# Optimization experiments

Hardware: AMD Instinct MI355X
Metric: run time of the kernel (lower is better)

The kernel has to match this reference:

```python
import jax, jax.numpy as jnp
import numpy as np

B, G, N_IN, N_HID, N_OUT = 2, 4096, 8, 32, 32
ALPHA, BETA, BN_EPS = 0.005, 5e-5, 1e-5
EDGE_P = 0.05  # adjacency density


def _lin_init(k, fan_in, fan_out):
    k1, k2 = jax.random.split(k)
    lim = 1.0 / np.sqrt(fan_in)
    W = jax.random.uniform(k1, (fan_in, fan_out), minval=-lim, maxval=lim, dtype=jnp.float32)
    b = jax.random.uniform(k2, (fan_out,), minval=-lim, maxval=lim, dtype=jnp.float32)
    return W, b


def setup_inputs() -> dict:
    key = jax.random.key(0)
    ks = jax.random.split(key, 12)
    W_infer, b_infer = _lin_init(ks[0], N_IN, N_HID)
    W_e1, b_e1 = _lin_init(ks[1], 2 * N_HID, 1)
    W_e2, b_e2 = _lin_init(ks[2], 2 * N_HID, 1)
    W_n1, b_n1 = _lin_init(ks[3], 2 * N_HID, N_OUT)
    W_n2, b_n2 = _lin_init(ks[4], 2 * N_HID, N_OUT)
    W_m1, b_m1 = _lin_init(ks[5], 2 * N_HID, N_OUT)
    W_m2, b_m2 = _lin_init(ks[6], 2 * N_HID, N_OUT)
    x = jax.random.normal(ks[7], (B, G, N_IN), dtype=jnp.float32)
    edges1 = jax.random.bernoulli(ks[8], EDGE_P, (G, G)).astype(jnp.float32)
    edges2 = jax.random.bernoulli(ks[9], EDGE_P, (G, G)).astype(jnp.float32)
    bn_gamma = jnp.ones((G,), jnp.float32)
    bn_beta = jnp.zeros((G,), jnp.float32)
    return dict(x=x, edges1=edges1, edges2=edges2, W_infer=W_infer, b_infer=b_infer,
                W_e1=W_e1, b_e1=b_e1, W_e2=W_e2, b_e2=b_e2,
                W_n1=W_n1, b_n1=b_n1, W_n2=W_n2, b_n2=b_n2,
                W_m1=W_m1, b_m1=b_m1, W_m2=W_m2, b_m2=b_m2,
                bn_gamma=bn_gamma, bn_beta=bn_beta)


def _mp_block(x, adj, coef, W_e, b_e, W_n, b_n, W_m, b_m):
    # x: [B,G,H]. Torch builds edge feature at flat index k=i*G+j as cat([x_j, x_i])
    # (shape2 = col gather, shape1 = row gather). We keep the same math without
    # materializing the [B,G*G,2H] tensor.
    Hh = x.shape[-1]
    s_src = x @ W_e[:Hh]   # [B,G,1]  (x_j part of mlp_edge)
    s_dst = x @ W_e[Hh:]   # [B,G,1]  (x_i part of mlp_edge)
    logits = s_dst[:, :, None, 0] + s_src[:, None, :, 0] + b_e[0]   # [B,G,G] at (i,j)
    w = adj + coef * (adj == 0).astype(x.dtype)                     # ori_edge + coef*thres_edge
    e = jax.nn.sigmoid(logits) * w[None]                            # [B,G,G]
    # receive at node i: sum_j e_ij * [x_j, x_i]
    recv_src = jnp.einsum('bij,bjh->bih', e, x)                     # sum_j e_ij x_j
    recv_dst = x * jnp.sum(e, axis=2)[..., None]                    # x_i * sum_j e_ij
    recv = jnp.concatenate([recv_src, recv_dst], axis=-1)           # [B,G,2H]
    recv = jax.nn.elu(recv @ W_n + b_n)                             # nodes_mlp + elu
    upd = jnp.concatenate([recv, x], axis=-1) @ W_m + b_m           # mesg_merge (mode='cat')
    return jax.nn.elu(upd)


def _forward(x, edges1, edges2, W_infer, b_infer, W_e1, b_e1, W_e2, b_e2,
             W_n1, b_n1, W_n2, b_n2, W_m1, b_m1, W_m2, b_m2, bn_gamma, bn_beta):
    h = jax.nn.elu(x @ W_infer + b_infer)                           # infer + elu, [B,G,H]
    h = _mp_block(h, edges1, ALPHA, W_e1, b_e1, W_n1, b_n1, W_m1, b_m1)
    # BatchNorm1d(gene_num) on [B, G, n_out]: per-gene stats over (batch, feature)
    mu = jnp.mean(h, axis=(0, 2), keepdims=True)
    var = jnp.var(h, axis=(0, 2), keepdims=True)
    h = (h - mu) * jax.lax.rsqrt(var + BN_EPS)
    h = h * bn_gamma[None, :, None] + bn_beta[None, :, None]
    return _mp_block(h, edges2, BETA, W_e2, b_e2, W_n2, b_n2, W_m2, b_m2)


def reference(x, edges1, edges2, W_infer, b_infer, W_e1, b_e1, W_e2, b_e2,
              W_n1, b_n1, W_n2, b_n2, W_m1, b_m1, W_m2, b_m2, bn_gamma, bn_beta):
    return _forward(x, edges1, edges2, W_infer, b_infer, W_e1, b_e1, W_e2, b_e2,
                    W_n1, b_n1, W_n2, b_n2, W_m1, b_m1, W_m2, b_m2, bn_gamma, bn_beta)
```

## Files before the change

### kernel.cpp

```cpp
#include <hip/hip_runtime.h>

#define G 4096
#define BSZ 2
#define NIN 8
#define HID 32
#define NLOG2E (-1.4426950408889634f)

typedef __attribute__((ext_vector_type(8))) short short8;
typedef __attribute__((ext_vector_type(4))) float floatx4;
typedef unsigned short ushort_t;
typedef unsigned int uint_t;

__device__ __forceinline__ float elu1(float v) {
    return v > 0.f ? v : (__expf(v) - 1.f);
}
__device__ __forceinline__ ushort_t f2bf(float f) {
    unsigned u = __float_as_uint(f);
    u += 0x7fffu + ((u >> 16) & 1u);
    return (ushort_t)(u >> 16);
}

__global__ __launch_bounds__(256) void k_setup1(
    const float* __restrict__ x, const float* __restrict__ W,
    const float* __restrict__ bias, const float* __restrict__ We,
    float* __restrict__ h0, ushort_t* __restrict__ hTb,
    float* __restrict__ ssrc, float* __restrict__ sdst) {
    __shared__ __align__(16) ushort_t hs[HID][264];
    int tid = threadIdx.x;
    int t = blockIdx.x * 256 + tid;
    int b = t >> 12;
    int g0 = (blockIdx.x & 15) * 256;
    float xin[NIN];
    const float* xp = x + t * NIN;
#pragma unroll
    for (int k = 0; k < NIN; k++) xin[k] = xp[k];
    float ss = 0.f, sd = 0.f;
    float* hp = h0 + (size_t)t * HID;
#pragma unroll
    for (int o = 0; o < HID; o++) {
        float v = bias[o];
#pragma unroll
        for (int k = 0; k < NIN; k++) v += xin[k] * W[k * HID + o];
        v = elu1(v);
        hp[o] = v;
        hs[o][tid] = f2bf(v);
        ss += v * We[o];
        sd += v * We[HID + o];
    }
    ssrc[t] = ss * NLOG2E;
    sdst[t] = sd * NLOG2E;
    __syncthreads();
#pragma unroll
    for (int p = 0; p < 4; p++) {
        int row = p * 8 + (tid >> 5);
        int c = (tid & 31) * 8;
        short8 v8 = *(const short8*)&hs[row][c];
        *(short8*)(void*)&hTb[(size_t)(b * HID + row) * G + g0 + c] = v8;
    }
}

template <bool DO_BN>
__global__ __launch_bounds__(1024, 4) void k_fused(
    const float* __restrict__ adj, const float* __restrict__ ssrc,
    const float* __restrict__ sdst, const ushort_t* __restrict__ hTb_in,
    const float* __restrict__ bep, float coef, const float* __restrict__ hin,
    const float* __restrict__ Wn, const float* __restrict__ bnb,
    const float* __restrict__ Wm, const float* __restrict__ bmb,
    const float* __restrict__ gamma, const float* __restrict__ beta,
    const float* __restrict__ We2, float* __restrict__ outp,
    ushort_t* __restrict__ hTb_out, float* __restrict__ s2s,
    float* __restrict__ s2d) {
    union SMemU {
        float ssm[BSZ][G];
        struct {
            float rec[32][68];
            float rec2[32][68];
            float esg[16][2];
            ushort_t tb[BSZ][HID][16];
        } p;
    };
    __shared__ __align__(16) SMemU sm;
    __shared__ __align__(16) uint_t abits[128][16];
    __shared__ __align__(16) float red[14][64][9];
    __shared__ __align__(16) float Wns[2048];
    __shared__ __align__(16) float Wms[2048];

    int tid = threadIdx.x;
    int g0 = blockIdx.x * 16;
    int l = tid & 63, w = tid >> 6;
    int b = w >> 3, jq = w & 7;

    if (tid < 512) {
        ((float4*)Wns)[tid] = ((const float4*)Wn)[tid];
    } else {
        int t2 = tid - 512;
        ((float4*)Wms)[t2] = ((const float4*)Wm)[t2];
    }
#pragma unroll
    for (int r = 0; r < 2; r++) {
        int idx = r * 4096 + tid * 4;
        int bb = idx >> 12, j = idx & 4095;
        *(float4*)&sm.ssm[bb][j] = *(const float4*)&ssrc[bb * G + j];
    }

    int m = l & 15, kg = l >> 4;
    int jstart = jq * 512;
    const ushort_t* hb0 = hTb_in + (size_t)(b * HID + m) * G + jstart + kg * 8;
    const ushort_t* hb1 = hb0 + (size_t)16 * G;
    short8 pb0[4], pb1[4];
#pragma unroll
    for (int d = 0; d < 4; d++) {
        pb0[d] = *(const short8*)(const void*)(hb0 + d * 32);
        pb1[d] = *(const short8*)(const void*)(hb1 + d * 32);
    }

    {
        int jw = tid >> 3;
        bool st = (tid & 7) == 0;
        int sh2 = (tid & 7) * 4;
        float4 ld[8];
#pragma unroll
        for (int h = 0; h < 2; h++) {
#pragma unroll
            for (int s = 0; s < 8; s++)
                ld[s] = *(const float4*)&adj[(size_t)(g0 + h * 8 + s) * G + tid * 4];
#pragma unroll
            for (int s = 0; s < 8; s++) {
                float4 v4 = ld[s];
                uint_t nib = (uint_t)(v4.x != 0.f) | ((uint_t)(v4.y != 0.f) << 1) |
                             ((uint_t)(v4.z != 0.f) << 2) | ((uint_t)(v4.w != 0.f) << 3);
                uint_t wd = nib << sh2;
                wd |= __shfl_xor(wd, 1);
                wd |= __shfl_xor(wd, 2);
                wd |= __shfl_xor(wd, 4);
                if (st) abits[jw][h * 8 + s] = wd;
            }
        }
    }

    float sd2 = sdst[b * G + g0 + m] + bep[0] * NLOG2E;
    const float wm1 = 1.f - coef;
    floatx4 c0 = {0.f, 0.f, 0.f, 0.f}, c1 = {0.f, 0.f, 0.f, 0.f};
    float es = 0.f;
    __syncthreads();

    const float* svp = &sm.ssm[b][jstart + kg * 8];
    const uint_t* abp = &abits[jq * 16][m];
    float4 sv0[2], sv1[2];
    uint_t bwr[2];
#pragma unroll
    for (int d = 0; d < 2; d++) {
        sv0[d] = *(const float4*)&svp[d * 32];
        sv1[d] = *(const float4*)&svp[d * 32 + 4];
        bwr[d] = abp[d * 16];
    }

#pragma unroll
    for (int jc = 0; jc < 16; jc++) {
        int pc = jc & 3, lc = jc & 1;
        short8 bf0 = pb0[pc], bf1 = pb1[pc];
        float4 s0 = sv0[lc], s1 = sv1[lc];
        uint_t bw = bwr[lc];
        if (jc + 4 < 16) {
            pb0[pc] = *(const short8*)(const void*)(hb0 + (jc + 4) * 32);
            pb1[pc] = *(const short8*)(const void*)(hb1 + (jc + 4) * 32);
        }
        if (jc + 2 < 16) {
            sv0[lc] = *(const float4*)&svp[(jc + 2) * 32];
            sv1[lc] = *(const float4*)&svp[(jc + 2) * 32 + 4];
            bwr[lc] = abp[(jc + 2) * 16];
        }
        float sv[8] = {s0.x, s0.y, s0.z, s0.w, s1.x, s1.y, s1.z, s1.w};
        short8 af;
#pragma unroll
        for (int t8 = 0; t8 < 8; t8++) {
            float bitf = (float)((bw >> (kg * 8 + t8)) & 1u);
            float wgt = __builtin_fmaf(bitf, wm1, coef);
            float ex = exp2f(sd2 + sv[t8]);
            float e = __builtin_amdgcn_rcpf(1.f + ex) * wgt;
            es += e;
            af[t8] = (short)f2bf(e);
        }
        c0 = __builtin_amdgcn_mfma_f32_16x16x32_bf16(af, bf0, c0, 0, 0, 0);
        c1 = __builtin_amdgcn_mfma_f32_16x16x32_bf16(af, bf1, c1, 0, 0, 0);
    }

    if (jq) {
        int widx = b * 7 + jq - 1;
#pragma unroll
        for (int r = 0; r < 4; r++) {
            red[widx][l][r] = c0[r];
            red[widx][l][4 + r] = c1[r];
        }
        red[widx][l][8] = es;
    }
    __syncthreads();
    if (!jq) {
#pragma unroll
        for (int q = 0; q < 7; q++) {
            int widx = b * 7 + q;
#pragma unroll
            for (int r = 0; r < 4; r++) {
                c0[r] += red[widx][l][r];
                c1[r] += red[widx][l][4 + r];
            }
            es += red[widx][l][8];
        }
        es += __shfl_xor(es, 16);
        es += __shfl_xor(es, 32);
#pragma unroll
        for (int r = 0; r < 4; r++) {
            int gene = (l >> 4) * 4 + r;
            sm.p.rec[gene * 2 + b][m] = c0[r];
            sm.p.rec[gene * 2 + b][16 + m] = c1[r];
        }
        if (l < 16) sm.p.esg[l][b] = es;
    }
    __syncthreads();

    int rl = tid >> 5, hh = tid & 31;
    int gene = rl >> 1, bb = rl & 1;
    float xv = hin[((size_t)(bb * G + g0 + gene)) * HID + hh];
    sm.p.rec[rl][32 + hh] = xv * sm.p.esg[gene][bb];
    __syncthreads();

    float v = bnb[hh];
#pragma unroll
    for (int k4 = 0; k4 < 16; k4++) {
        float4 r4 = *(const float4*)&sm.p.rec[rl][k4 * 4];
        v += r4.x * Wns[(k4 * 4 + 0) * HID + hh];
        v += r4.y * Wns[(k4 * 4 + 1) * HID + hh];
        v += r4.z * Wns[(k4 * 4 + 2) * HID + hh];
        v += r4.w * Wns[(k4 * 4 + 3) * HID + hh];
    }
    v = elu1(v);
    sm.p.rec2[rl][hh] = v;
    sm.p.rec2[rl][32 + hh] = xv;
    float u = bmb[hh];
#pragma unroll
    for (int k4 = 0; k4 < 16; k4++) {
        float4 r4 = *(const float4*)&sm.p.rec2[rl][k4 * 4];
        u += r4.x * Wms[(k4 * 4 + 0) * HID + hh];
        u += r4.y * Wms[(k4 * 4 + 1) * HID + hh];
        u += r4.z * Wms[(k4 * 4 + 2) * HID + hh];
        u += r4.w * Wms[(k4 * 4 + 3) * HID + hh];
    }
    float h1v = elu1(u);
    if (!DO_BN) {
        outp[((size_t)(bb * G + g0 + gene)) * HID + hh] = h1v;
    } else {
        float s = h1v, sq = h1v * h1v;
#pragma unroll
        for (int mm = 32; mm; mm >>= 1) {
            s += __shfl_xor(s, mm);
            sq += __shfl_xor(sq, mm);
        }
        float mu = s * (1.f / 64.f);
        float var = sq * (1.f / 64.f) - mu * mu;
        float rstd = rsqrtf(var + 1e-5f);
        float hn = (h1v - mu) * rstd * gamma[g0 + gene] + beta[g0 + gene];
        outp[((size_t)(bb * G + g0 + gene)) * HID + hh] = hn;
        sm.p.tb[bb][hh][gene] = f2bf(hn);
        float ps = hn * We2[hh], pd = hn * We2[HID + hh];
#pragma unroll
        for (int mm = 16; mm; mm >>= 1) {
            ps += __shfl_xor(ps, mm);
            pd += __shfl_xor(pd, mm);
        }
        if (hh == 0) {
            s2s[bb * G + g0 + gene] = ps * NLOG2E;
            s2d[bb * G + g0 + gene] = pd * NLOG2E;
        }
        __syncthreads();
        if (tid < 128) {
            int b2 = tid >> 6, c = (tid >> 1) & 31, half = tid & 1;
            short8 v8 = *(const short8*)&sm.p.tb[b2][c][half * 8];
            *(short8*)(void*)&hTb_out[(size_t)(b2 * HID + c) * G + g0 + half * 8] = v8;
        }
    }
}

extern "C" void kernel_launch(void* const* d_in, const int* in_sizes, int n_in,
                              void* d_out, int out_size, void* d_ws, size_t ws_size,
                              hipStream_t stream) {
    const float* x      = (const float*)d_in[0];
    const float* edges1 = (const float*)d_in[1];
    const float* edges2 = (const float*)d_in[2];
    const float* W_inf  = (const float*)d_in[3];
    const float* b_inf  = (const float*)d_in[4];
    const float* W_e1   = (const float*)d_in[5];
    const float* b_e1   = (const float*)d_in[6];
    const float* W_e2   = (const float*)d_in[7];
    const float* b_e2   = (const float*)d_in[8];
    const float* W_n1   = (const float*)d_in[9];
    const float* b_n1   = (const float*)d_in[10];
    const float* W_n2   = (const float*)d_in[11];
    const float* b_n2   = (const float*)d_in[12];
    const float* W_m1   = (const float*)d_in[13];
    const float* b_m1   = (const float*)d_in[14];
    const float* W_m2   = (const float*)d_in[15];
    const float* b_m2   = (const float*)d_in[16];
    const float* bn_g   = (const float*)d_in[17];
    const float* bn_b   = (const float*)d_in[18];
    float* out = (float*)d_out;

    float* ws = (float*)d_ws;
    float* h0   = ws;
    float* h1n  = ws + 262144;
    float* s1s  = ws + 524288;
    float* s1d  = ws + 532480;
    float* s2s  = ws + 540672;
    float* s2d  = ws + 548864;
    ushort_t* hTb  = (ushort_t*)(ws + 557056);
    ushort_t* hTb2 = (ushort_t*)(ws + 688128);

    const float ALPHA = 0.005f, BETA = 5e-5f;

    k_setup1<<<32, 256, 0, stream>>>(x, W_inf, b_inf, W_e1, h0, hTb, s1s, s1d);
    k_fused<true><<<G / 16, 1024, 0, stream>>>(
        edges1, s1s, s1d, hTb, b_e1, ALPHA, h0, W_n1, b_n1, W_m1, b_m1,
        bn_g, bn_b, W_e2, h1n, hTb2, s2s, s2d);
    k_fused<false><<<G / 16, 1024, 0, stream>>>(
        edges2, s2s, s2d, hTb2, b_e2, BETA, h1n, W_n2, b_n2, W_m2, b_m2,
        nullptr, nullptr, nullptr, out, nullptr, nullptr, nullptr);
}
```

Before: 239.8 us.

## Prepack both adjacency matrices into bitmasks in a separate kernel

Adds a k_prepack kernel that turns both float adjacency matrices into 32-bit bitmask words in one pass. The fused kernels then read these packed words (128 per row) instead of loading and packing float rows with shuffles. The bitmask shared-memory array is padded to a stride of 17 to avoid bank conflicts on the new transposed stores. The full float adjacency is still read once, now in a separate launch, so the saving comes from better parallelism and removing the shuffle reductions from the serial fused kernels, at the cost of an extra launch and workspace.

```diff
diff --git a/kernel.cpp b/kernel.cpp
--- a/kernel.cpp
+++ b/kernel.cpp
@@ -59,9 +59,28 @@
     }
 }
 
+__global__ __launch_bounds__(256) void k_prepack(
+    const float* __restrict__ e1, const float* __restrict__ e2,
+    uint_t* __restrict__ pk1, uint_t* __restrict__ pk2) {
+    int bi = blockIdx.x;
+    const float* src = (bi < 2048) ? e1 : e2;
+    uint_t* dst = (bi < 2048) ? pk1 : pk2;
+    int idx = (bi & 2047) * 256 + threadIdx.x;
+    const float* p = src + (size_t)idx * 32;
+    uint_t wd = 0;
+#pragma unroll
+    for (int q = 0; q < 8; q++) {
+        float4 v4 = *(const float4*)(p + q * 4);
+        uint_t nib = (uint_t)(v4.x != 0.f) | ((uint_t)(v4.y != 0.f) << 1) |
+                     ((uint_t)(v4.z != 0.f) << 2) | ((uint_t)(v4.w != 0.f) << 3);
+        wd |= nib << (q * 4);
+    }
+    dst[idx] = wd;
+}
+
 template <bool DO_BN>
 __global__ __launch_bounds__(1024, 4) void k_fused(
-    const float* __restrict__ adj, const float* __restrict__ ssrc,
+    const uint_t* __restrict__ pk, const float* __restrict__ ssrc,
     const float* __restrict__ sdst, const ushort_t* __restrict__ hTb_in,
     const float* __restrict__ bep, float coef, const float* __restrict__ hin,
     const float* __restrict__ Wn, const float* __restrict__ bnb,
@@ -80,7 +99,7 @@
         } p;
     };
     __shared__ __align__(16) SMemU sm;
-    __shared__ __align__(16) uint_t abits[128][16];
+    __shared__ __align__(16) uint_t abits[128][17];
     __shared__ __align__(16) float red[14][64][9];
     __shared__ __align__(16) float Wns[2048];
     __shared__ __align__(16) float Wms[2048];
@@ -89,6 +108,9 @@
     int g0 = blockIdx.x * 16;
     int l = tid & 63, w = tid >> 6;
     int b = w >> 3, jq = w & 7;
+
+    uint_t w0 = pk[g0 * 128 + tid];
+    uint_t w1 = pk[g0 * 128 + 1024 + tid];
 
     if (tid < 512) {
         ((float4*)Wns)[tid] = ((const float4*)Wn)[tid];
@@ -114,29 +136,8 @@
         pb1[d] = *(const short8*)(const void*)(hb1 + d * 32);
     }
 
-    {
-        int jw = tid >> 3;
-        bool st = (tid & 7) == 0;
-        int sh2 = (tid & 7) * 4;
-        float4 ld[8];
-#pragma unroll
-        for (int h = 0; h < 2; h++) {
-#pragma unroll
-            for (int s = 0; s < 8; s++)
-                ld[s] = *(const float4*)&adj[(size_t)(g0 + h * 8 + s) * G + tid * 4];
-#pragma unroll
-            for (int s = 0; s < 8; s++) {
-                float4 v4 = ld[s];
-                uint_t nib = (uint_t)(v4.x != 0.f) | ((uint_t)(v4.y != 0.f) << 1) |
-                             ((uint_t)(v4.z != 0.f) << 2) | ((uint_t)(v4.w != 0.f) << 3);
-                uint_t wd = nib << sh2;
-                wd |= __shfl_xor(wd, 1);
-                wd |= __shfl_xor(wd, 2);
-                wd |= __shfl_xor(wd, 4);
-                if (st) abits[jw][h * 8 + s] = wd;
-            }
-        }
-    }
+    abits[tid & 127][tid >> 7] = w0;
+    abits[tid & 127][(tid >> 7) + 8] = w1;
 
     float sd2 = sdst[b * G + g0 + m] + bep[0] * NLOG2E;
     const float wm1 = 1.f - coef;
@@ -152,7 +153,7 @@
     for (int d = 0; d < 2; d++) {
         sv0[d] = *(const float4*)&svp[d * 32];
         sv1[d] = *(const float4*)&svp[d * 32 + 4];
-        bwr[d] = abp[d * 16];
+        bwr[d] = abp[d * 17];
     }
 
 #pragma unroll
@@ -168,7 +169,7 @@
         if (jc + 2 < 16) {
             sv0[lc] = *(const float4*)&svp[(jc + 2) * 32];
             sv1[lc] = *(const float4*)&svp[(jc + 2) * 32 + 4];
-            bwr[lc] = abp[(jc + 2) * 16];
+            bwr[lc] = abp[(jc + 2) * 17];
         }
         float sv[8] = {s0.x, s0.y, s0.z, s0.w, s1.x, s1.y, s1.z, s1.w};
         short8 af;
@@ -313,14 +314,17 @@
     float* s2d  = ws + 548864;
     ushort_t* hTb  = (ushort_t*)(ws + 557056);
     ushort_t* hTb2 = (ushort_t*)(ws + 688128);
+    uint_t* pk1 = (uint_t*)(ws + 819200);
+    uint_t* pk2 = pk1 + 524288;
 
     const float ALPHA = 0.005f, BETA = 5e-5f;
 
     k_setup1<<<32, 256, 0, stream>>>(x, W_inf, b_inf, W_e1, h0, hTb, s1s, s1d);
+    k_prepack<<<4096, 256, 0, stream>>>(edges1, edges2, pk1, pk2);
     k_fused<true><<<G / 16, 1024, 0, stream>>>(
-        edges1, s1s, s1d, hTb, b_e1, ALPHA, h0, W_n1, b_n1, W_m1, b_m1,
+        pk1, s1s, s1d, hTb, b_e1, ALPHA, h0, W_n1, b_n1, W_m1, b_m1,
         bn_g, bn_b, W_e2, h1n, hTb2, s2s, s2d);
     k_fused<false><<<G / 16, 1024, 0, stream>>>(
-        edges2, s2s, s2d, hTb2, b_e2, BETA, h1n, W_n2, b_n2, W_m2, b_m2,
+        pk2, s2s, s2d, hTb2, b_e2, BETA, h1n, W_n2, b_n2, W_m2, b_m2,
         nullptr, nullptr, nullptr, out, nullptr, nullptr, nullptr);
 }
```

Measured after the change: 245.0 us. 2.2% more time.

## Halve fused-kernel block to 512 threads with 4 warps per batch over longer j ranges

Applied to the files above, without the earlier changes.

Shrinks the fused message-passing block from 1024 to 512 threads, so each wave covers 1024 j columns (32 MFMA steps) instead of 512. This cuts the cross-wave reduction buffer to 6 slots and remaps the adjacency bit-pack and the node MLP epilogue so each thread handles two rows. It also pads the abits shared array to avoid bank conflicts and replaces round-to-nearest bf16 conversion with truncation for the edge weights. The goal is less reduction and sync overhead plus more blocks resident per CU, at the cost of longer serial loops per wave and slightly less precise bf16 edge weights.

```diff
diff --git a/kernel.cpp b/kernel.cpp
--- a/kernel.cpp
+++ b/kernel.cpp
@@ -60,7 +60,7 @@
 }
 
 template <bool DO_BN>
-__global__ __launch_bounds__(1024, 4) void k_fused(
+__global__ __launch_bounds__(512, 4) void k_fused(
     const float* __restrict__ adj, const float* __restrict__ ssrc,
     const float* __restrict__ sdst, const ushort_t* __restrict__ hTb_in,
     const float* __restrict__ bep, float coef, const float* __restrict__ hin,
@@ -80,60 +80,60 @@
         } p;
     };
     __shared__ __align__(16) SMemU sm;
-    __shared__ __align__(16) uint_t abits[128][16];
-    __shared__ __align__(16) float red[14][64][9];
+    __shared__ __align__(16) uint_t abits[128][17];
+    __shared__ __align__(16) float red[6][64][9];
     __shared__ __align__(16) float Wns[2048];
     __shared__ __align__(16) float Wms[2048];
 
     int tid = threadIdx.x;
     int g0 = blockIdx.x * 16;
     int l = tid & 63, w = tid >> 6;
-    int b = w >> 3, jq = w & 7;
-
-    if (tid < 512) {
-        ((float4*)Wns)[tid] = ((const float4*)Wn)[tid];
-    } else {
-        int t2 = tid - 512;
-        ((float4*)Wms)[t2] = ((const float4*)Wm)[t2];
-    }
-#pragma unroll
-    for (int r = 0; r < 2; r++) {
-        int idx = r * 4096 + tid * 4;
+    int b = w >> 2, jq = w & 3;
+
+    ((float4*)Wns)[tid] = ((const float4*)Wn)[tid];
+    ((float4*)Wms)[tid] = ((const float4*)Wm)[tid];
+#pragma unroll
+    for (int r = 0; r < 4; r++) {
+        int idx = r * 2048 + tid * 4;
         int bb = idx >> 12, j = idx & 4095;
         *(float4*)&sm.ssm[bb][j] = *(const float4*)&ssrc[bb * G + j];
     }
 
     int m = l & 15, kg = l >> 4;
-    int jstart = jq * 512;
+    int jstart = jq * 1024;
     const ushort_t* hb0 = hTb_in + (size_t)(b * HID + m) * G + jstart + kg * 8;
     const ushort_t* hb1 = hb0 + (size_t)16 * G;
-    short8 pb0[4], pb1[4];
-#pragma unroll
-    for (int d = 0; d < 4; d++) {
+    short8 pb0[2], pb1[2];
+#pragma unroll
+    for (int d = 0; d < 2; d++) {
         pb0[d] = *(const short8*)(const void*)(hb0 + d * 32);
         pb1[d] = *(const short8*)(const void*)(hb1 + d * 32);
     }
 
     {
-        int jw = tid >> 3;
-        bool st = (tid & 7) == 0;
-        int sh2 = (tid & 7) * 4;
-        float4 ld[8];
-#pragma unroll
-        for (int h = 0; h < 2; h++) {
-#pragma unroll
-            for (int s = 0; s < 8; s++)
-                ld[s] = *(const float4*)&adj[(size_t)(g0 + h * 8 + s) * G + tid * 4];
-#pragma unroll
-            for (int s = 0; s < 8; s++) {
-                float4 v4 = ld[s];
+        const int sh2 = (tid & 7) * 4;
+        const bool st = (tid & 7) == 0;
+        const int wbase = tid >> 3;
+        float4 ld[4];
+#pragma unroll
+        for (int bt = 0; bt < 8; bt++) {
+            int r0 = bt * 2;
+#pragma unroll
+            for (int q = 0; q < 4; q++) {
+                int r = r0 + (q >> 1), h = q & 1;
+                ld[q] = *(const float4*)&adj[(size_t)(g0 + r) * G + (h * 512 + tid) * 4];
+            }
+#pragma unroll
+            for (int q = 0; q < 4; q++) {
+                int r = r0 + (q >> 1), h = q & 1;
+                float4 v4 = ld[q];
                 uint_t nib = (uint_t)(v4.x != 0.f) | ((uint_t)(v4.y != 0.f) << 1) |
                              ((uint_t)(v4.z != 0.f) << 2) | ((uint_t)(v4.w != 0.f) << 3);
                 uint_t wd = nib << sh2;
                 wd |= __shfl_xor(wd, 1);
                 wd |= __shfl_xor(wd, 2);
                 wd |= __shfl_xor(wd, 4);
-                if (st) abits[jw][h * 8 + s] = wd;
+                if (st) abits[h * 64 + wbase][r] = wd;
             }
         }
     }
@@ -145,30 +145,27 @@
     __syncthreads();
 
     const float* svp = &sm.ssm[b][jstart + kg * 8];
-    const uint_t* abp = &abits[jq * 16][m];
     float4 sv0[2], sv1[2];
     uint_t bwr[2];
 #pragma unroll
     for (int d = 0; d < 2; d++) {
         sv0[d] = *(const float4*)&svp[d * 32];
         sv1[d] = *(const float4*)&svp[d * 32 + 4];
-        bwr[d] = abp[d * 16];
-    }
-
-#pragma unroll
-    for (int jc = 0; jc < 16; jc++) {
-        int pc = jc & 3, lc = jc & 1;
-        short8 bf0 = pb0[pc], bf1 = pb1[pc];
+        bwr[d] = abits[jq * 32 + d][m];
+    }
+
+#pragma unroll 4
+    for (int jc = 0; jc < 32; jc++) {
+        int lc = jc & 1;
+        short8 bf0 = pb0[lc], bf1 = pb1[lc];
         float4 s0 = sv0[lc], s1 = sv1[lc];
         uint_t bw = bwr[lc];
-        if (jc + 4 < 16) {
-            pb0[pc] = *(const short8*)(const void*)(hb0 + (jc + 4) * 32);
-            pb1[pc] = *(const short8*)(const void*)(hb1 + (jc + 4) * 32);
-        }
-        if (jc + 2 < 16) {
+        if (jc + 2 < 32) {
+            pb0[lc] = *(const short8*)(const void*)(hb0 + (jc + 2) * 32);
+            pb1[lc] = *(const short8*)(const void*)(hb1 + (jc + 2) * 32);
             sv0[lc] = *(const float4*)&svp[(jc + 2) * 32];
             sv1[lc] = *(const float4*)&svp[(jc + 2) * 32 + 4];
-            bwr[lc] = abp[(jc + 2) * 16];
+            bwr[lc] = abits[jq * 32 + jc + 2][m];
         }
         float sv[8] = {s0.x, s0.y, s0.z, s0.w, s1.x, s1.y, s1.z, s1.w};
         short8 af;
@@ -179,14 +176,14 @@
             float ex = exp2f(sd2 + sv[t8]);
             float e = __builtin_amdgcn_rcpf(1.f + ex) * wgt;
             es += e;
-            af[t8] = (short)f2bf(e);
+            af[t8] = (short)(__float_as_uint(e) >> 16);
         }
         c0 = __builtin_amdgcn_mfma_f32_16x16x32_bf16(af, bf0, c0, 0, 0, 0);
         c1 = __builtin_amdgcn_mfma_f32_16x16x32_bf16(af, bf1, c1, 0, 0, 0);
     }
 
     if (jq) {
-        int widx = b * 7 + jq - 1;
+        int widx = b * 3 + jq - 1;
 #pragma unroll
         for (int r = 0; r < 4; r++) {
             red[widx][l][r] = c0[r];
@@ -197,8 +194,8 @@
     __syncthreads();
     if (!jq) {
 #pragma unroll
-        for (int q = 0; q < 7; q++) {
-            int widx = b * 7 + q;
+        for (int q = 0; q < 3; q++) {
+            int widx = b * 3 + q;
 #pragma unroll
             for (int r = 0; r < 4; r++) {
                 c0[r] += red[widx][l][r];
@@ -219,58 +216,68 @@
     __syncthreads();
 
     int rl = tid >> 5, hh = tid & 31;
-    int gene = rl >> 1, bb = rl & 1;
-    float xv = hin[((size_t)(bb * G + g0 + gene)) * HID + hh];
-    sm.p.rec[rl][32 + hh] = xv * sm.p.esg[gene][bb];
-    __syncthreads();
-
-    float v = bnb[hh];
-#pragma unroll
-    for (int k4 = 0; k4 < 16; k4++) {
-        float4 r4 = *(const float4*)&sm.p.rec[rl][k4 * 4];
-        v += r4.x * Wns[(k4 * 4 + 0) * HID + hh];
-        v += r4.y * Wns[(k4 * 4 + 1) * HID + hh];
-        v += r4.z * Wns[(k4 * 4 + 2) * HID + hh];
-        v += r4.w * Wns[(k4 * 4 + 3) * HID + hh];
-    }
-    v = elu1(v);
-    sm.p.rec2[rl][hh] = v;
-    sm.p.rec2[rl][32 + hh] = xv;
-    float u = bmb[hh];
-#pragma unroll
-    for (int k4 = 0; k4 < 16; k4++) {
-        float4 r4 = *(const float4*)&sm.p.rec2[rl][k4 * 4];
-        u += r4.x * Wms[(k4 * 4 + 0) * HID + hh];
-        u += r4.y * Wms[(k4 * 4 + 1) * HID + hh];
-        u += r4.z * Wms[(k4 * 4 + 2) * HID + hh];
-        u += r4.w * Wms[(k4 * 4 + 3) * HID + hh];
-    }
-    float h1v = elu1(u);
-    if (!DO_BN) {
-        outp[((size_t)(bb * G + g0 + gene)) * HID + hh] = h1v;
-    } else {
-        float s = h1v, sq = h1v * h1v;
-#pragma unroll
-        for (int mm = 32; mm; mm >>= 1) {
-            s += __shfl_xor(s, mm);
-            sq += __shfl_xor(sq, mm);
-        }
-        float mu = s * (1.f / 64.f);
-        float var = sq * (1.f / 64.f) - mu * mu;
-        float rstd = rsqrtf(var + 1e-5f);
-        float hn = (h1v - mu) * rstd * gamma[g0 + gene] + beta[g0 + gene];
-        outp[((size_t)(bb * G + g0 + gene)) * HID + hh] = hn;
-        sm.p.tb[bb][hh][gene] = f2bf(hn);
-        float ps = hn * We2[hh], pd = hn * We2[HID + hh];
-#pragma unroll
-        for (int mm = 16; mm; mm >>= 1) {
-            ps += __shfl_xor(ps, mm);
-            pd += __shfl_xor(pd, mm);
-        }
-        if (hh == 0) {
-            s2s[bb * G + g0 + gene] = ps * NLOG2E;
-            s2d[bb * G + g0 + gene] = pd * NLOG2E;
-        }
+    float xv[2];
+#pragma unroll
+    for (int p = 0; p < 2; p++) {
+        int rr = rl + p * 16, gene = rr >> 1, bb = rr & 1;
+        xv[p] = hin[((size_t)(bb * G + g0 + gene)) * HID + hh];
+        sm.p.rec[rr][32 + hh] = xv[p] * sm.p.esg[gene][bb];
+    }
+    __syncthreads();
+
+#pragma unroll
+    for (int p = 0; p < 2; p++) {
+        int rr = rl + p * 16, gene = rr >> 1, bb = rr & 1;
+        float v = bnb[hh];
+#pragma unroll
+        for (int k4 = 0; k4 < 16; k4++) {
+            float4 r4 = *(const float4*)&sm.p.rec[rr][k4 * 4];
+            v += r4.x * Wns[(k4 * 4 + 0) * HID + hh];
+            v += r4.y * Wns[(k4 * 4 + 1) * HID + hh];
+            v += r4.z * Wns[(k4 * 4 + 2) * HID + hh];
+            v += r4.w * Wns[(k4 * 4 + 3) * HID + hh];
+        }
+        v = elu1(v);
+        sm.p.rec2[rr][hh] = v;
+        sm.p.rec2[rr][32 + hh] = xv[p];
+        float u = bmb[hh];
+#pragma unroll
+        for (int k4 = 0; k4 < 16; k4++) {
+            float4 r4 = *(const float4*)&sm.p.rec2[rr][k4 * 4];
+            u += r4.x * Wms[(k4 * 4 + 0) * HID + hh];
+            u += r4.y * Wms[(k4 * 4 + 1) * HID + hh];
+            u += r4.z * Wms[(k4 * 4 + 2) * HID + hh];
+            u += r4.w * Wms[(k4 * 4 + 3) * HID + hh];
+        }
+        float h1v = elu1(u);
+        if (!DO_BN) {
+            outp[((size_t)(bb * G + g0 + gene)) * HID + hh] = h1v;
+        } else {
+            float s = h1v, sq = h1v * h1v;
+#pragma unroll
+            for (int mm = 32; mm; mm >>= 1) {
+                s += __shfl_xor(s, mm);
+                sq += __shfl_xor(sq, mm);
+            }
+            float mu = s * (1.f / 64.f);
+            float var = sq * (1.f / 64.f) - mu * mu;
+            float rstd = rsqrtf(var + 1e-5f);
+            float hn = (h1v - mu) * rstd * gamma[g0 + gene] + beta[g0 + gene];
+            outp[((size_t)(bb * G + g0 + gene)) * HID + hh] = hn;
+            sm.p.tb[bb][hh][gene] = f2bf(hn);
+            float ps = hn * We2[hh], pd = hn * We2[HID + hh];
+#pragma unroll
+            for (int mm = 16; mm; mm >>= 1) {
+                ps += __shfl_xor(ps, mm);
+                pd += __shfl_xor(pd, mm);
+            }
+            if (hh == 0) {
+                s2s[bb * G + g0 + gene] = ps * NLOG2E;
+                s2d[bb * G + g0 + gene] = pd * NLOG2E;
+            }
+        }
+    }
+    if (DO_BN) {
         __syncthreads();
         if (tid < 128) {
             int b2 = tid >> 6, c = (tid >> 1) & 31, half = tid & 1;
@@ -317,10 +324,10 @@
     const float ALPHA = 0.005f, BETA = 5e-5f;
 
     k_setup1<<<32, 256, 0, stream>>>(x, W_inf, b_inf, W_e1, h0, hTb, s1s, s1d);
-    k_fused<true><<<G / 16, 1024, 0, stream>>>(
+    k_fused<true><<<G / 16, 512, 0, stream>>>(
         edges1, s1s, s1d, hTb, b_e1, ALPHA, h0, W_n1, b_n1, W_m1, b_m1,
         bn_g, bn_b, W_e2, h1n, hTb2, s2s, s2d);
-    k_fused<false><<<G / 16, 1024, 0, stream>>>(
+    k_fused<false><<<G / 16, 512, 0, stream>>>(
         edges2, s2s, s2d, hTb2, b_e2, BETA, h1n, W_n2, b_n2, W_m2, b_m2,
         nullptr, nullptr, nullptr, out, nullptr, nullptr, nullptr);
 }
```

Result: slower. 253.7 us (+5.8%).
